# Kernel tuning notes

Hardware: AMD Instinct MI355X
Metric: run time of the kernel (lower is better)

## Reference

```python
import jax, jax.numpy as jnp
import numpy as np

DIM = 1024
NE = 4            # num_experts
MLP = 4           # mlp_ratio
H = 16            # num_heads
HD = DIM // H     # head dim
EXP = 3 * DIM + MLP * DIM   # expand output dim (7*dim)
CIN = DIM + MLP * DIM       # contract input dim (5*dim)


def layer_norm(x, g, b, eps=1e-5):
    m = jnp.mean(x, axis=-1, keepdims=True)
    v = jnp.var(x, axis=-1, keepdims=True)
    return (x - m) * jax.lax.rsqrt(v + eps) * g + b


def setup_inputs() -> dict:
    key = jax.random.key(0)
    ks = jax.random.split(key, 8)
    B, N = 8, 1024
    x = jax.random.normal(ks[0], (B, N, DIM), jnp.float32)
    expert_mask = jax.random.randint(ks[1], (B, N), 0, NE, jnp.int32)
    router_probs = jax.random.uniform(ks[2], (B, N, NE), jnp.float32)
    expand_weight = jax.random.normal(ks[3], (EXP, DIM), jnp.float32) * 0.02
    mlp_bias = jnp.zeros((MLP * DIM,), jnp.float32)
    contract_weight = jax.random.normal(ks[4], (2 * DIM, CIN), jnp.float32) * 0.02
    contract_bias = jnp.zeros((2 * DIM,), jnp.float32)
    norm1_g = jnp.ones((DIM,), jnp.float32)
    norm1_b = jnp.zeros((DIM,), jnp.float32)
    norm2_g = jnp.ones((DIM,), jnp.float32)
    norm2_b = jnp.zeros((DIM,), jnp.float32)
    alpha = jnp.zeros((1,), jnp.float32)
    return dict(x=x, expert_mask=expert_mask, router_probs=router_probs,
                expand_weight=expand_weight, mlp_bias=mlp_bias,
                contract_weight=contract_weight, contract_bias=contract_bias,
                norm1_g=norm1_g, norm1_b=norm1_b, norm2_g=norm2_g, norm2_b=norm2_b,
                alpha=alpha)


def reference(x, expert_mask, router_probs, expand_weight, mlp_bias,
              contract_weight, contract_bias, norm1_g, norm1_b,
              norm2_g, norm2_b, alpha):
    B, N, _ = x.shape
    shift = (NE - 1 - expert_mask).astype(jnp.int32)          # [B,N]
    # nested (matryoshka) active dims per token
    d_in = DIM // jnp.left_shift(1, shift)                    # expand: active input dims
    d_out = (2 * DIM) // jnp.left_shift(1, shift)             # contract: active output dims

    # nested_linear_expand: zero inactive input features, then full GEMM
    in_mask = (jnp.arange(DIM) < d_in[..., None]).astype(x.dtype)
    xn = layer_norm(x, norm1_g, norm1_b) * in_mask
    y = jnp.einsum('bnd,od->bno', xn, expand_weight)          # [B,N,7*dim]

    qkv = y[..., :3 * DIM]
    mlp_hidden = y[..., 3 * DIM:] + mlp_bias

    q = qkv[..., :DIM]
    k = layer_norm(qkv[..., DIM:2 * DIM], norm2_g, norm2_b)
    v = layer_norm(qkv[..., 2 * DIM:], norm2_g, norm2_b)

    qh = q.reshape(B, N, H, HD)
    kh = k.reshape(B, N, H, HD)
    vh = v.reshape(B, N, H, HD)
    scale = HD ** -0.5
    attn = jax.nn.softmax(jnp.einsum('bqhd,bkhd->bhqk', qh, kh) * scale, axis=-1)
    attn_out = jnp.einsum('bhqk,bkhd->bqhd', attn, vh).reshape(B, N, DIM)

    h = jnp.concatenate([attn_out, jax.nn.gelu(mlp_hidden, approximate=False)], axis=-1)
    # nested_linear_contract: full GEMM, zero inactive output features
    z = jnp.einsum('bnc,oc->bno', h, contract_weight) + contract_bias  # [B,N,2*dim]
    z = z * (jnp.arange(2 * DIM) < d_out[..., None]).astype(z.dtype)

    attn_o = z[..., :DIM] + x
    mlp_o = z[..., DIM:]
    expert_probs = jnp.take_along_axis(router_probs, expert_mask[..., None].astype(jnp.int32), axis=-1)  # [B,N,1]
    out = attn_o + (alpha * expert_probs + 1.0) * mlp_o
    return (out, expert_mask, router_probs)
```

## Files before the change

kernel.cpp:

```cpp
#include <hip/hip_runtime.h>
#include <hip/hip_bf16.h>
#include <math.h>

typedef __bf16 bf16_t;
typedef __attribute__((ext_vector_type(8))) __bf16 bf16x8;
typedef __attribute__((ext_vector_type(4))) __bf16 bf16x4;
typedef __attribute__((ext_vector_type(4))) float f32x4;

typedef __attribute__((address_space(1))) unsigned as1u;
typedef __attribute__((address_space(3))) unsigned as3u;

#define MAXT1 68
#define MAXJ2 1056

__device__ __forceinline__ void async_copy16(bf16_t* lds, const bf16_t* g) {
  __builtin_amdgcn_global_load_lds((as1u*)g, (as3u*)lds, 16, 0, 0);
}

__device__ __forceinline__ float gelu_exact(float t) {
  return 0.5f * t * (1.0f + erff(t * 0.70710678118654752f));
}

__global__ __launch_bounds__(256)
void cast_kernel(const float* __restrict__ w, bf16_t* __restrict__ o, int n) {
  int i = (blockIdx.x * 256 + threadIdx.x) * 4;
  if (i < n) {
    float4 v = *(const float4*)(w + i);
    bf16x4 t;
    t[0] = (bf16_t)v.x; t[1] = (bf16_t)v.y; t[2] = (bf16_t)v.z; t[3] = (bf16_t)v.w;
    *(bf16x4*)(o + i) = t;
  }
}

__global__ __launch_bounds__(1024)
void sort_kernel(const int* __restrict__ em, int* __restrict__ perm,
                 int* __restrict__ t1, int* __restrict__ j2) {
  __shared__ int cnt[4], cur[4], tb[5], jb[5];
  const int tid = threadIdx.x;
  const int wave = tid >> 6, lane = tid & 63;
  if (tid < 4) cnt[tid] = 0;
  __syncthreads();
  for (int c = wave; c < 128; c += 16) {
    int e = em[c * 64 + lane];
    unsigned long long m0 = __ballot(e == 0), m1 = __ballot(e == 1);
    unsigned long long m2 = __ballot(e == 2), m3 = __ballot(e == 3);
    if (lane == 0) {
      atomicAdd(&cnt[0], (int)__popcll(m0)); atomicAdd(&cnt[1], (int)__popcll(m1));
      atomicAdd(&cnt[2], (int)__popcll(m2)); atomicAdd(&cnt[3], (int)__popcll(m3));
    }
  }
  __syncthreads();
  if (tid == 0) {
    cur[0] = 0; cur[1] = cnt[0]; cur[2] = cnt[0] + cnt[1]; cur[3] = cnt[0] + cnt[1] + cnt[2];
    tb[0] = 0; jb[0] = 0;
    for (int e = 0; e < 4; ++e) {
      int nt = (cnt[e] + 127) >> 7;
      tb[e + 1] = tb[e] + nt;
      jb[e + 1] = jb[e] + nt * (2 << e);
    }
  }
  __syncthreads();
  for (int c = wave; c < 128; c += 16) {
    int i = c * 64 + lane;
    int e = em[i];
    unsigned long long m0 = __ballot(e == 0), m1 = __ballot(e == 1);
    unsigned long long m2 = __ballot(e == 2), m3 = __ballot(e == 3);
    unsigned long long me = e == 0 ? m0 : e == 1 ? m1 : e == 2 ? m2 : m3;
    int bl = 0;
    if (lane < 4) {
      unsigned long long ml = lane == 0 ? m0 : lane == 1 ? m1 : lane == 2 ? m2 : m3;
      bl = atomicAdd(&cur[lane], (int)__popcll(ml));
    }
    int base = __shfl(bl, e);
    unsigned long long lt = (1ull << lane) - 1ull;
    perm[base + (int)__popcll(me & lt)] = i;
  }
  int offp[5];
  offp[0] = 0;
  #pragma unroll
  for (int e = 0; e < 4; ++e) offp[e + 1] = offp[e] + cnt[e];
  for (int t = tid; t < MAXT1; t += 1024) {
    int e = -1, loc = 0;
    #pragma unroll
    for (int q = 0; q < 4; ++q) if (t >= tb[q] && t < tb[q + 1]) { e = q; loc = t - tb[q]; }
    if (e >= 0) {
      t1[t * 3] = e; t1[t * 3 + 1] = offp[e] + loc * 128;
      t1[t * 3 + 2] = min(128, cnt[e] - loc * 128);
    } else t1[t * 3] = -1;
  }
  for (int j = tid; j < MAXJ2; j += 1024) {
    int e = -1, loc = 0;
    #pragma unroll
    for (int q = 0; q < 4; ++q) if (j >= jb[q] && j < jb[q + 1]) { e = q; loc = j - jb[q]; }
    if (e >= 0) {
      int t = loc >> (1 + e), b = loc & ((2 << e) - 1);
      j2[j * 4] = e; j2[j * 4 + 1] = offp[e] + t * 128;
      j2[j * 4 + 2] = min(128, cnt[e] - t * 128); j2[j * 4 + 3] = b;
    } else j2[j * 4] = -1;
  }
}

__global__ __launch_bounds__(256)
void ln1_kernel(const float* __restrict__ x, const float* __restrict__ gam,
                const float* __restrict__ bet, const int* __restrict__ em,
                bf16_t* __restrict__ xn) {
  const int row = blockIdx.x, tid = threadIdx.x;
  const float4 v = ((const float4*)(x + (size_t)row * 1024))[tid];
  float s = v.x + v.y + v.z + v.w;
  float sq = v.x * v.x + v.y * v.y + v.z * v.z + v.w * v.w;
  #pragma unroll
  for (int off = 1; off < 64; off <<= 1) { s += __shfl_xor(s, off); sq += __shfl_xor(sq, off); }
  __shared__ float red[8];
  const int wave = tid >> 6, lane = tid & 63;
  if (lane == 0) { red[wave] = s; red[4 + wave] = sq; }
  __syncthreads();
  s = red[0] + red[1] + red[2] + red[3];
  sq = red[4] + red[5] + red[6] + red[7];
  const float mean = s * (1.0f / 1024.0f);
  const float var = sq * (1.0f / 1024.0f) - mean * mean;
  const float rstd = rsqrtf(var + 1e-5f);
  const int din = 1024 >> (3 - em[row]);
  const float4 gv = ((const float4*)gam)[tid];
  const float4 bv = ((const float4*)bet)[tid];
  const int c0 = tid * 4;
  float vf[4] = {v.x, v.y, v.z, v.w};
  float gf[4] = {gv.x, gv.y, gv.z, gv.w};
  float bvf[4] = {bv.x, bv.y, bv.z, bv.w};
  bf16x4 o;
  #pragma unroll
  for (int i = 0; i < 4; ++i) {
    float t = (vf[i] - mean) * rstd * gf[i] + bvf[i];
    o[i] = (c0 + i < din) ? (bf16_t)t : (bf16_t)0.0f;
  }
  *(bf16x4*)(xn + (size_t)row * 1024 + c0) = o;
}

__global__ __launch_bounds__(256)
void ln2_kernel(bf16_t* __restrict__ kv, const float* __restrict__ gam,
                const float* __restrict__ bet) {
  const int row = blockIdx.x, tid = threadIdx.x;
  bf16_t* base = kv + (size_t)row * 2048;
  bf16x4 kk = *(const bf16x4*)(base + tid * 4);
  bf16x4 vv = *(const bf16x4*)(base + 1024 + tid * 4);
  float kf[4], vf[4];
  float ks = 0, ksq = 0, vs = 0, vsq = 0;
  #pragma unroll
  for (int i = 0; i < 4; ++i) {
    kf[i] = (float)kk[i]; ks += kf[i]; ksq += kf[i] * kf[i];
    vf[i] = (float)vv[i]; vs += vf[i]; vsq += vf[i] * vf[i];
  }
  #pragma unroll
  for (int off = 1; off < 64; off <<= 1) {
    ks += __shfl_xor(ks, off); ksq += __shfl_xor(ksq, off);
    vs += __shfl_xor(vs, off); vsq += __shfl_xor(vsq, off);
  }
  __shared__ float red[16];
  const int wave = tid >> 6, lane = tid & 63;
  if (lane == 0) { red[wave] = ks; red[4 + wave] = ksq; red[8 + wave] = vs; red[12 + wave] = vsq; }
  __syncthreads();
  ks = red[0] + red[1] + red[2] + red[3];
  ksq = red[4] + red[5] + red[6] + red[7];
  vs = red[8] + red[9] + red[10] + red[11];
  vsq = red[12] + red[13] + red[14] + red[15];
  const float mk = ks * (1.f / 1024.f), mv = vs * (1.f / 1024.f);
  const float rk = rsqrtf(ksq * (1.f / 1024.f) - mk * mk + 1e-5f);
  const float rv = rsqrtf(vsq * (1.f / 1024.f) - mv * mv + 1e-5f);
  const float4 gv = ((const float4*)gam)[tid];
  const float4 bv = ((const float4*)bet)[tid];
  float gf[4] = {gv.x, gv.y, gv.z, gv.w}, bvf[4] = {bv.x, bv.y, bv.z, bv.w};
  bf16x4 ko, vo;
  #pragma unroll
  for (int i = 0; i < 4; ++i) {
    ko[i] = (bf16_t)((kf[i] - mk) * rk * gf[i] + bvf[i]);
    vo[i] = (bf16_t)((vf[i] - mv) * rv * gf[i] + bvf[i]);
  }
  *(bf16x4*)(base + tid * 4) = ko;
  *(bf16x4*)(base + 1024 + tid * 4) = vo;
}

template<int EPI>
__global__ __launch_bounds__(256)
void gemm_bt(const bf16_t* __restrict__ A, const bf16_t* __restrict__ W,
             const int* __restrict__ perm, const int* __restrict__ desc,
             const float* __restrict__ bias,
             bf16_t* __restrict__ hb, bf16_t* __restrict__ kvb,
             float* __restrict__ z_attn, bf16_t* __restrict__ z_mlp) {
  constexpr int K = (EPI == 0) ? 1024 : 5120;
  const int* d = desc + blockIdx.x * ((EPI == 0) ? 3 : 4);
  const int e = d[0];
  if (e < 0) return;
  const int nval = d[2];
  const int bn = (EPI == 0) ? blockIdx.y : d[3];
  const int nkt = (EPI == 0) ? (2 << e) : 80;

  __shared__ bf16_t As[128 * 64];
  __shared__ bf16_t Bs[128 * 64];
  __shared__ int prow[128];
  const int tid = threadIdx.x;
  if (tid < 128) prow[tid] = perm[d[1] + min(tid, nval - 1)];
  const int wave = tid >> 6, lane = tid & 63;
  const int l15 = lane & 15, l4 = lane >> 4;
  const int wm = wave >> 1, wn = wave & 1;

  f32x4 acc[4][4] = {};

  const int rbase = tid >> 3;
  const int ss = (tid & 7) ^ (rbase & 7);
  __syncthreads();
  const bf16_t* Ag[4];
  #pragma unroll
  for (int i = 0; i < 4; ++i) Ag[i] = A + (size_t)prow[i * 32 + rbase] * K + ss * 8;
  const bf16_t* Wg = W + (size_t)(bn * 128 + rbase) * K + ss * 8;

  for (int kt = 0; kt < nkt; ++kt) {
    #pragma unroll
    for (int i = 0; i < 4; ++i) {
      async_copy16(As + (i * 256 + wave * 64) * 8, Ag[i] + kt * 64);
      async_copy16(Bs + (i * 256 + wave * 64) * 8, Wg + (size_t)i * 32 * K + kt * 64);
    }
    __syncthreads();
    #pragma unroll
    for (int ks = 0; ks < 2; ++ks) {
      bf16x8 a[4], b[4];
      #pragma unroll
      for (int mi = 0; mi < 4; ++mi) {
        const int r = wm * 64 + mi * 16 + l15;
        const int slot = (ks * 4 + l4) ^ (r & 7);
        a[mi] = *(const bf16x8*)(As + r * 64 + slot * 8);
      }
      #pragma unroll
      for (int ni = 0; ni < 4; ++ni) {
        const int r = wn * 64 + ni * 16 + l15;
        const int slot = (ks * 4 + l4) ^ (r & 7);
        b[ni] = *(const bf16x8*)(Bs + r * 64 + slot * 8);
      }
      #pragma unroll
      for (int mi = 0; mi < 4; ++mi)
        #pragma unroll
        for (int ni = 0; ni < 4; ++ni)
          acc[mi][ni] = __builtin_amdgcn_mfma_f32_16x16x32_bf16(a[mi], b[ni], acc[mi][ni], 0, 0, 0);
    }
    __syncthreads();
  }

  #pragma unroll
  for (int mi = 0; mi < 4; ++mi) {
    #pragma unroll
    for (int ni = 0; ni < 4; ++ni) {
      const int gc = bn * 128 + wn * 64 + ni * 16 + l15;
      #pragma unroll
      for (int r = 0; r < 4; ++r) {
        const int gml = wm * 64 + mi * 16 + l4 * 4 + r;
        if (gml < nval) {
          const size_t token = (size_t)prow[gml];
          const float c = acc[mi][ni][r];
          if (EPI == 0) {
            if (gc < 1024) {
              hb[token * 5120 + gc] = (bf16_t)c;
            } else if (gc < 3072) {
              kvb[token * 2048 + (gc - 1024)] = (bf16_t)c;
            } else {
              const float t = c + bias[gc - 3072];
              hb[token * 5120 + 1024 + (gc - 3072)] = (bf16_t)gelu_exact(t);
            }
          } else {
            const float t = c + bias[gc];
            if (gc < 1024) z_attn[token * 1024 + gc] = t;
            else           z_mlp[token * 1024 + (gc - 1024)] = (bf16_t)t;
          }
        }
      }
    }
  }
}

__global__ __launch_bounds__(256)
void attn_kernel(const bf16_t* __restrict__ kv, bf16_t* __restrict__ hb) {
  __shared__ bf16_t Kl[64 * 64];
  __shared__ bf16_t Vt[64 * 72];
  __shared__ bf16_t Pl[4][16 * 72];
  const int tid = threadIdx.x;
  const int wave = tid >> 6, lane = tid & 63;
  const int l15 = lane & 15, l4 = lane >> 4;
  const int qt = blockIdx.x, bh = blockIdx.y;
  const int bb = bh >> 4, head = bh & 15;
  const int tok0 = bb << 10;
  const int d0 = head << 6;

  const int qrow = tok0 + qt * 64 + wave * 16 + l15;
  const bf16x8 aq0 = *(const bf16x8*)(hb + (size_t)qrow * 5120 + d0 + l4 * 8);
  const bf16x8 aq1 = *(const bf16x8*)(hb + (size_t)qrow * 5120 + d0 + 32 + l4 * 8);

  f32x4 o[4] = {};
  float mrun[4] = {-1e30f, -1e30f, -1e30f, -1e30f};
  float lrun[4] = {0.f, 0.f, 0.f, 0.f};

  const int krb = tid >> 3;
  const int kss = (tid & 7) ^ (krb & 7);

  for (int kt = 0; kt < 16; ++kt) {
    const int krow0 = tok0 + kt * 64;
    #pragma unroll
    for (int i = 0; i < 2; ++i) {
      const int r = i * 32 + krb;
      async_copy16(Kl + (i * 256 + wave * 64) * 8,
                   kv + (size_t)(krow0 + r) * 2048 + d0 + kss * 8);
    }
    #pragma unroll
    for (int i = 0; i < 2; ++i) {
      const int key = i * 32 + (tid >> 3);
      const int dc = tid & 7;
      bf16x8 vvv = *(const bf16x8*)(kv + (size_t)(krow0 + key) * 2048 + 1024 + d0 + dc * 8);
      #pragma unroll
      for (int j = 0; j < 8; ++j) Vt[(dc * 8 + j) * 72 + key] = vvv[j];
    }
    __syncthreads();

    f32x4 s[4] = {};
    #pragma unroll
    for (int ks = 0; ks < 2; ++ks) {
      const bf16x8 aqk = ks ? aq1 : aq0;
      #pragma unroll
      for (int kc = 0; kc < 4; ++kc) {
        const int r = kc * 16 + l15;
        const int slot = (ks * 4 + l4) ^ (r & 7);
        bf16x8 bk = *(const bf16x8*)(Kl + r * 64 + slot * 8);
        s[kc] = __builtin_amdgcn_mfma_f32_16x16x32_bf16(aqk, bk, s[kc], 0, 0, 0);
      }
    }
    #pragma unroll
    for (int r = 0; r < 4; ++r) {
      float mx = -1e30f;
      #pragma unroll
      for (int kc = 0; kc < 4; ++kc) mx = fmaxf(mx, s[kc][r]);
      mx = fmaxf(mx, __shfl_xor(mx, 1));
      mx = fmaxf(mx, __shfl_xor(mx, 2));
      mx = fmaxf(mx, __shfl_xor(mx, 4));
      mx = fmaxf(mx, __shfl_xor(mx, 8));
      mx *= 0.125f;
      const float mnew = fmaxf(mrun[r], mx);
      const float corr = __expf(mrun[r] - mnew);
      float ps = 0.f;
      #pragma unroll
      for (int kc = 0; kc < 4; ++kc) {
        const float p = __expf(s[kc][r] * 0.125f - mnew);
        ps += p;
        Pl[wave][(l4 * 4 + r) * 72 + kc * 16 + l15] = (bf16_t)p;
      }
      ps += __shfl_xor(ps, 1); ps += __shfl_xor(ps, 2);
      ps += __shfl_xor(ps, 4); ps += __shfl_xor(ps, 8);
      lrun[r] = lrun[r] * corr + ps;
      mrun[r] = mnew;
      o[0][r] *= corr; o[1][r] *= corr; o[2][r] *= corr; o[3][r] *= corr;
    }
    const bf16x8 ap0 = *(const bf16x8*)(&Pl[wave][l15 * 72 + l4 * 8]);
    const bf16x8 ap1 = *(const bf16x8*)(&Pl[wave][l15 * 72 + 32 + l4 * 8]);
    #pragma unroll
    for (int dn = 0; dn < 4; ++dn) {
      const int r = dn * 16 + l15;
      bf16x8 bv0 = *(const bf16x8*)(Vt + r * 72 + l4 * 8);
      bf16x8 bv1 = *(const bf16x8*)(Vt + r * 72 + 32 + l4 * 8);
      o[dn] = __builtin_amdgcn_mfma_f32_16x16x32_bf16(ap0, bv0, o[dn], 0, 0, 0);
      o[dn] = __builtin_amdgcn_mfma_f32_16x16x32_bf16(ap1, bv1, o[dn], 0, 0, 0);
    }
    __syncthreads();
  }

  #pragma unroll
  for (int r = 0; r < 4; ++r) {
    const float inv = 1.0f / lrun[r];
    const int gq = tok0 + qt * 64 + wave * 16 + l4 * 4 + r;
    #pragma unroll
    for (int dn = 0; dn < 4; ++dn)
      hb[(size_t)gq * 5120 + d0 + dn * 16 + l15] = (bf16_t)(o[dn][r] * inv);
  }
}

__global__ __launch_bounds__(256)
void final_kernel(const float* __restrict__ z_attn, const bf16_t* __restrict__ z_mlp,
                  const float* __restrict__ x, const int* __restrict__ em,
                  const float* __restrict__ rp, const float* __restrict__ alpha,
                  float* __restrict__ out) {
  const int row = blockIdx.x, tid = threadIdx.x;
  const int e = em[row];
  const int dout = 2048 >> (3 - e);
  const float f = alpha[0] * rp[row * 4 + e] + 1.0f;
  const float4 z0 = ((const float4*)(z_attn + (size_t)row * 1024))[tid];
  const bf16x4 z1 = ((const bf16x4*)(z_mlp + (size_t)row * 1024))[tid];
  const float4 xv = ((const float4*)(x + (size_t)row * 1024))[tid];
  const int c = tid * 4;
  float4 o;
  o.x = ((c + 0) < dout ? z0.x : 0.f) + xv.x + f * ((1024 + c + 0) < dout ? (float)z1[0] : 0.f);
  o.y = ((c + 1) < dout ? z0.y : 0.f) + xv.y + f * ((1024 + c + 1) < dout ? (float)z1[1] : 0.f);
  o.z = ((c + 2) < dout ? z0.z : 0.f) + xv.z + f * ((1024 + c + 2) < dout ? (float)z1[2] : 0.f);
  o.w = ((c + 3) < dout ? z0.w : 0.f) + xv.w + f * ((1024 + c + 3) < dout ? (float)z1[3] : 0.f);
  ((float4*)(out + (size_t)row * 1024))[tid] = o;
  float* out_em = out + 8388608;
  float* out_rp = out_em + 8192;
  if (tid == 0) out_em[row] = (float)e;
  if (tid < 4) out_rp[row * 4 + tid] = rp[row * 4 + tid];
}

extern "C" void kernel_launch(void* const* d_in, const int* in_sizes, int n_in,
                              void* d_out, int out_size, void* d_ws, size_t ws_size,
                              hipStream_t stream) {
  const float* x = (const float*)d_in[0];
  const int* em = (const int*)d_in[1];
  const float* rp = (const float*)d_in[2];
  const float* w_exp = (const float*)d_in[3];
  const float* mlp_bias = (const float*)d_in[4];
  const float* w_con = (const float*)d_in[5];
  const float* c_bias = (const float*)d_in[6];
  const float* n1g = (const float*)d_in[7];
  const float* n1b = (const float*)d_in[8];
  const float* n2g = (const float*)d_in[9];
  const float* n2b = (const float*)d_in[10];
  const float* alpha = (const float*)d_in[11];

  char* ws = (char*)d_ws;
  bf16_t* Wexp  = (bf16_t*)ws;
  bf16_t* xn    = (bf16_t*)(ws + 14680064);
  bf16_t* z_mlp = (bf16_t*)(ws + 14680064);
  int*    perm  = (int*)(ws + 31457280);
  int*    t1d   = (int*)(ws + 31457280 + 32768);
  int*    j2d   = (int*)(ws + 31457280 + 34816);
  bf16_t* kvb   = (bf16_t*)(ws + 48234496);
  float*  z_att = (float*)(ws + 48234496);
  bf16_t* Wcon  = (bf16_t*)(ws + 81788928);
  bf16_t* hb    = (bf16_t*)(ws + 102760448);

  sort_kernel<<<1, 1024, 0, stream>>>(em, perm, t1d, j2d);
  cast_kernel<<<7168, 256, 0, stream>>>(w_exp, Wexp, 7340032);
  cast_kernel<<<10240, 256, 0, stream>>>(w_con, Wcon, 10485760);
  ln1_kernel<<<8192, 256, 0, stream>>>(x, n1g, n1b, em, xn);
  gemm_bt<0><<<dim3(MAXT1, 56), 256, 0, stream>>>(xn, Wexp, perm, t1d, mlp_bias,
                                                  hb, kvb, nullptr, nullptr);
  ln2_kernel<<<8192, 256, 0, stream>>>(kvb, n2g, n2b);
  attn_kernel<<<dim3(16, 128), 256, 0, stream>>>(kvb, hb);
  gemm_bt<1><<<MAXJ2, 256, 0, stream>>>(hb, Wcon, perm, j2d, c_bias,
                                        nullptr, nullptr, z_att, z_mlp);
  final_kernel<<<8192, 256, 0, stream>>>(z_att, z_mlp, x, em, rp, alpha, (float*)d_out);
}
```

Before: 488.3 us.

## Pre-transpose V and keep softmax probabilities in registers via bpermute

```diff
diff --git a/kernel.cpp b/kernel.cpp
--- a/kernel.cpp
+++ b/kernel.cpp
@@ -6,6 +6,7 @@
 typedef __attribute__((ext_vector_type(8))) __bf16 bf16x8;
 typedef __attribute__((ext_vector_type(4))) __bf16 bf16x4;
 typedef __attribute__((ext_vector_type(4))) float f32x4;
+typedef __attribute__((ext_vector_type(4))) unsigned u32x4;
 
 typedef __attribute__((address_space(1))) unsigned as1u;
 typedef __attribute__((address_space(3))) unsigned as3u;
@@ -19,6 +20,12 @@
 
 __device__ __forceinline__ float gelu_exact(float t) {
   return 0.5f * t * (1.0f + erff(t * 0.70710678118654752f));
+}
+
+__device__ __forceinline__ unsigned pack_bf16(float a, float b) {
+  unsigned short ha = __builtin_bit_cast(unsigned short, (bf16_t)a);
+  unsigned short hb = __builtin_bit_cast(unsigned short, (bf16_t)b);
+  return (unsigned)ha | ((unsigned)hb << 16);
 }
 
 __global__ __launch_bounds__(256)
@@ -176,6 +183,30 @@
   }
   *(bf16x4*)(base + tid * 4) = ko;
   *(bf16x4*)(base + 1024 + tid * 4) = vo;
+}
+
+__global__ __launch_bounds__(256)
+void vt_kernel(const bf16_t* __restrict__ kv, bf16_t* __restrict__ vT) {
+  __shared__ bf16_t t[64][80];
+  const int tt = blockIdx.x, head = blockIdx.y;
+  const int tid = threadIdx.x;
+  const int r8 = tid >> 3, c8 = tid & 7;
+  #pragma unroll
+  for (int i = 0; i < 2; ++i) {
+    const int tok = i * 32 + r8;
+    bf16x8 v = *(const bf16x8*)(kv + (size_t)(tt * 64 + tok) * 2048 + 1024 + head * 64 + c8 * 8);
+    #pragma unroll
+    for (int j = 0; j < 8; ++j) t[c8 * 8 + j][tok] = v[j];
+  }
+  __syncthreads();
+  const int bb = tt >> 4;
+  const int tloc = (tt & 15) * 64;
+  #pragma unroll
+  for (int i = 0; i < 2; ++i) {
+    const int d = i * 32 + r8;
+    bf16x8 v = *(const bf16x8*)(&t[d][c8 * 8]);
+    *(bf16x8*)(vT + (size_t)((bb * 16 + head) * 64 + d) * 1024 + tloc + c8 * 8) = v;
+  }
 }
 
 template<int EPI>
@@ -275,104 +306,133 @@
 }
 
 __global__ __launch_bounds__(256)
-void attn_kernel(const bf16_t* __restrict__ kv, bf16_t* __restrict__ hb) {
+void attn_kernel(const bf16_t* __restrict__ kv, const bf16_t* __restrict__ vT,
+                 bf16_t* __restrict__ hb) {
   __shared__ bf16_t Kl[64 * 64];
-  __shared__ bf16_t Vt[64 * 72];
-  __shared__ bf16_t Pl[4][16 * 72];
+  __shared__ bf16_t Vl[64 * 64];
   const int tid = threadIdx.x;
   const int wave = tid >> 6, lane = tid & 63;
   const int l15 = lane & 15, l4 = lane >> 4;
   const int qt = blockIdx.x, bh = blockIdx.y;
-  const int bb = bh >> 4, head = bh & 15;
+  const int bb = bh >> 4;
   const int tok0 = bb << 10;
-  const int d0 = head << 6;
+  const int d0 = (bh & 15) << 6;
 
   const int qrow = tok0 + qt * 64 + wave * 16 + l15;
-  const bf16x8 aq0 = *(const bf16x8*)(hb + (size_t)qrow * 5120 + d0 + l4 * 8);
-  const bf16x8 aq1 = *(const bf16x8*)(hb + (size_t)qrow * 5120 + d0 + 32 + l4 * 8);
+  const bf16x8 bq0 = *(const bf16x8*)(hb + (size_t)qrow * 5120 + d0 + l4 * 8);
+  const bf16x8 bq1 = *(const bf16x8*)(hb + (size_t)qrow * 5120 + d0 + 32 + l4 * 8);
 
   f32x4 o[4] = {};
-  float mrun[4] = {-1e30f, -1e30f, -1e30f, -1e30f};
-  float lrun[4] = {0.f, 0.f, 0.f, 0.f};
+  float mrun = -1e30f, lrun = 0.f;
 
   const int krb = tid >> 3;
   const int kss = (tid & 7) ^ (krb & 7);
+  const int idx0 = ((2 * (l4 & 1) + 0) * 16 + l15) * 4;
+  const int idx1 = ((2 * (l4 & 1) + 1) * 16 + l15) * 4;
+  const bool hi = (l4 >> 1) != 0;
 
   for (int kt = 0; kt < 16; ++kt) {
     const int krow0 = tok0 + kt * 64;
     #pragma unroll
     for (int i = 0; i < 2; ++i) {
-      const int r = i * 32 + krb;
       async_copy16(Kl + (i * 256 + wave * 64) * 8,
-                   kv + (size_t)(krow0 + r) * 2048 + d0 + kss * 8);
-    }
-    #pragma unroll
-    for (int i = 0; i < 2; ++i) {
-      const int key = i * 32 + (tid >> 3);
-      const int dc = tid & 7;
-      bf16x8 vvv = *(const bf16x8*)(kv + (size_t)(krow0 + key) * 2048 + 1024 + d0 + dc * 8);
-      #pragma unroll
-      for (int j = 0; j < 8; ++j) Vt[(dc * 8 + j) * 72 + key] = vvv[j];
+                   kv + (size_t)(krow0 + i * 32 + krb) * 2048 + d0 + kss * 8);
+      async_copy16(Vl + (i * 256 + wave * 64) * 8,
+                   vT + (size_t)(bh * 64 + i * 32 + krb) * 1024 + kt * 64 + kss * 8);
     }
     __syncthreads();
 
     f32x4 s[4] = {};
     #pragma unroll
     for (int ks = 0; ks < 2; ++ks) {
-      const bf16x8 aqk = ks ? aq1 : aq0;
+      const bf16x8 bq = ks ? bq1 : bq0;
       #pragma unroll
       for (int kc = 0; kc < 4; ++kc) {
         const int r = kc * 16 + l15;
         const int slot = (ks * 4 + l4) ^ (r & 7);
-        bf16x8 bk = *(const bf16x8*)(Kl + r * 64 + slot * 8);
-        s[kc] = __builtin_amdgcn_mfma_f32_16x16x32_bf16(aqk, bk, s[kc], 0, 0, 0);
+        bf16x8 ak = *(const bf16x8*)(Kl + r * 64 + slot * 8);
+        s[kc] = __builtin_amdgcn_mfma_f32_16x16x32_bf16(ak, bq, s[kc], 0, 0, 0);
       }
     }
-    #pragma unroll
-    for (int r = 0; r < 4; ++r) {
-      float mx = -1e30f;
-      #pragma unroll
-      for (int kc = 0; kc < 4; ++kc) mx = fmaxf(mx, s[kc][r]);
-      mx = fmaxf(mx, __shfl_xor(mx, 1));
-      mx = fmaxf(mx, __shfl_xor(mx, 2));
-      mx = fmaxf(mx, __shfl_xor(mx, 4));
-      mx = fmaxf(mx, __shfl_xor(mx, 8));
-      mx *= 0.125f;
-      const float mnew = fmaxf(mrun[r], mx);
-      const float corr = __expf(mrun[r] - mnew);
-      float ps = 0.f;
-      #pragma unroll
-      for (int kc = 0; kc < 4; ++kc) {
+
+    float mx = s[0][0];
+    #pragma unroll
+    for (int kc = 0; kc < 4; ++kc)
+      #pragma unroll
+      for (int r = 0; r < 4; ++r) mx = fmaxf(mx, s[kc][r]);
+    mx = fmaxf(mx, __shfl_xor(mx, 16));
+    mx = fmaxf(mx, __shfl_xor(mx, 32));
+    mx *= 0.125f;
+    const float mnew = fmaxf(mrun, mx);
+    const float corr = __expf(mrun - mnew);
+    float ps = 0.f;
+    #pragma unroll
+    for (int kc = 0; kc < 4; ++kc)
+      #pragma unroll
+      for (int r = 0; r < 4; ++r) {
         const float p = __expf(s[kc][r] * 0.125f - mnew);
+        s[kc][r] = p;
         ps += p;
-        Pl[wave][(l4 * 4 + r) * 72 + kc * 16 + l15] = (bf16_t)p;
       }
-      ps += __shfl_xor(ps, 1); ps += __shfl_xor(ps, 2);
-      ps += __shfl_xor(ps, 4); ps += __shfl_xor(ps, 8);
-      lrun[r] = lrun[r] * corr + ps;
-      mrun[r] = mnew;
-      o[0][r] *= corr; o[1][r] *= corr; o[2][r] *= corr; o[3][r] *= corr;
-    }
-    const bf16x8 ap0 = *(const bf16x8*)(&Pl[wave][l15 * 72 + l4 * 8]);
-    const bf16x8 ap1 = *(const bf16x8*)(&Pl[wave][l15 * 72 + 32 + l4 * 8]);
+    ps += __shfl_xor(ps, 16);
+    ps += __shfl_xor(ps, 32);
+    lrun = lrun * corr + ps;
+    mrun = mnew;
+
+    unsigned pd[4][2], bp[4][2][2];
+    #pragma unroll
+    for (int kc = 0; kc < 4; ++kc) {
+      pd[kc][0] = pack_bf16(s[kc][0], s[kc][1]);
+      pd[kc][1] = pack_bf16(s[kc][2], s[kc][3]);
+    }
+    #pragma unroll
+    for (int kc = 0; kc < 4; ++kc)
+      #pragma unroll
+      for (int rp = 0; rp < 2; ++rp) {
+        bp[kc][rp][0] = (unsigned)__builtin_amdgcn_ds_bpermute(idx0, (int)pd[kc][rp]);
+        bp[kc][rp][1] = (unsigned)__builtin_amdgcn_ds_bpermute(idx1, (int)pd[kc][rp]);
+      }
+    u32x4 w0, w1;
+    w0[0] = hi ? bp[1][0][0] : bp[0][0][0];
+    w0[1] = hi ? bp[1][1][0] : bp[0][1][0];
+    w0[2] = hi ? bp[1][0][1] : bp[0][0][1];
+    w0[3] = hi ? bp[1][1][1] : bp[0][1][1];
+    w1[0] = hi ? bp[3][0][0] : bp[2][0][0];
+    w1[1] = hi ? bp[3][1][0] : bp[2][1][0];
+    w1[2] = hi ? bp[3][0][1] : bp[2][0][1];
+    w1[3] = hi ? bp[3][1][1] : bp[2][1][1];
+    const bf16x8 pa0 = __builtin_bit_cast(bf16x8, w0);
+    const bf16x8 pa1 = __builtin_bit_cast(bf16x8, w1);
+
+    float cq[4];
+    #pragma unroll
+    for (int r = 0; r < 4; ++r) cq[r] = __shfl(corr, l4 * 4 + r);
+    #pragma unroll
+    for (int dn = 0; dn < 4; ++dn)
+      #pragma unroll
+      for (int r = 0; r < 4; ++r) o[dn][r] *= cq[r];
+
     #pragma unroll
     for (int dn = 0; dn < 4; ++dn) {
       const int r = dn * 16 + l15;
-      bf16x8 bv0 = *(const bf16x8*)(Vt + r * 72 + l4 * 8);
-      bf16x8 bv1 = *(const bf16x8*)(Vt + r * 72 + 32 + l4 * 8);
-      o[dn] = __builtin_amdgcn_mfma_f32_16x16x32_bf16(ap0, bv0, o[dn], 0, 0, 0);
-      o[dn] = __builtin_amdgcn_mfma_f32_16x16x32_bf16(ap1, bv1, o[dn], 0, 0, 0);
+      bf16x8 bv0 = *(const bf16x8*)(Vl + r * 64 + ((l4 ^ (r & 7)) * 8));
+      bf16x8 bv1 = *(const bf16x8*)(Vl + r * 64 + (((4 + l4) ^ (r & 7)) * 8));
+      o[dn] = __builtin_amdgcn_mfma_f32_16x16x32_bf16(pa0, bv0, o[dn], 0, 0, 0);
+      o[dn] = __builtin_amdgcn_mfma_f32_16x16x32_bf16(pa1, bv1, o[dn], 0, 0, 0);
     }
     __syncthreads();
   }
 
+  const float il = 1.0f / lrun;
+  float linv[4];
+  #pragma unroll
+  for (int r = 0; r < 4; ++r) linv[r] = __shfl(il, l4 * 4 + r);
   #pragma unroll
   for (int r = 0; r < 4; ++r) {
-    const float inv = 1.0f / lrun[r];
     const int gq = tok0 + qt * 64 + wave * 16 + l4 * 4 + r;
     #pragma unroll
     for (int dn = 0; dn < 4; ++dn)
-      hb[(size_t)gq * 5120 + d0 + dn * 16 + l15] = (bf16_t)(o[dn][r] * inv);
+      hb[(size_t)gq * 5120 + d0 + dn * 16 + l15] = (bf16_t)(o[dn][r] * linv[r]);
   }
 }
 
@@ -420,6 +480,7 @@
   char* ws = (char*)d_ws;
   bf16_t* Wexp  = (bf16_t*)ws;
   bf16_t* xn    = (bf16_t*)(ws + 14680064);
+  bf16_t* vT    = (bf16_t*)(ws + 14680064);
   bf16_t* z_mlp = (bf16_t*)(ws + 14680064);
   int*    perm  = (int*)(ws + 31457280);
   int*    t1d   = (int*)(ws + 31457280 + 32768);
@@ -436,7 +497,8 @@
   gemm_bt<0><<<dim3(MAXT1, 56), 256, 0, stream>>>(xn, Wexp, perm, t1d, mlp_bias,
                                                   hb, kvb, nullptr, nullptr);
   ln2_kernel<<<8192, 256, 0, stream>>>(kvb, n2g, n2b);
-  attn_kernel<<<dim3(16, 128), 256, 0, stream>>>(kvb, hb);
+  vt_kernel<<<dim3(128, 16), 256, 0, stream>>>(kvb, vT);
+  attn_kernel<<<dim3(16, 128), 256, 0, stream>>>(kvb, vT, hb);
   gemm_bt<1><<<MAXJ2, 256, 0, stream>>>(hb, Wcon, perm, j2d, c_bias,
                                         nullptr, nullptr, z_att, z_mlp);
   final_kernel<<<8192, 256, 0, stream>>>(z_att, z_mlp, x, em, rp, alpha, (float*)d_out);
```

After: 426.1 us. 12.7% less time.
